# Kernel tuning notes

Measured on AMD Instinct MI355X. Metric: run time of the kernel, lower is better.

## Reference

```python
import jax, jax.numpy as jnp
import numpy as np
from jax import lax

BETA = 1.0
EPS_BIS = 0.1   # eps_threshold of FIND_MIN
N_ITER = 24     # enough bisection steps for any interval width seen here
N_BOX = 2097152
TINY = 1e-12


def _slog(x):
    return jnp.log(jnp.maximum(x, TINY))


def _sl1(x):  # smooth_l1_loss
    d = jnp.abs(x)
    return jnp.where(d < BETA, 0.5 * d * d / BETA, d - 0.5 * BETA)


def _sl1p(x):  # smooth_l1_loss_prime
    return jnp.clip(x / BETA, -1.0, 1.0)


def _xi_prime(w, wp, wh):
    return 0.5 * _sl1p(0.5 * (w - wh)) + _sl1p(_slog(w) - _slog(wp)) / jnp.maximum(w, TINY)


def _sigma(w, wp, wh):
    return w * _xi_prime(w, wp, wh)


def _xi(w, wp, wh):  # bbox_loss at x=(w-wh)/2
    return _sl1(0.5 * (w - wh)) + _sl1(_slog(wp) - _slog(w))


def _bisect(u, v, f):
    # vectorized FIND_MIN: early-exit endpoints + bisection to width < EPS_BIS
    fu, fv = f(u), f(v)

    def body(i, c):
        lo, hi = c
        act = (hi - lo) >= EPS_BIS
        m = 0.5 * (lo + hi)
        pos = f(m) >= 0
        lo = jnp.where(act & ~pos, m, lo)
        hi = jnp.where(act & pos, m, hi)
        return lo, hi

    lo, hi = lax.fori_loop(0, N_ITER, body, (u, v))
    m = 0.5 * (lo + hi)
    return jnp.where(fu >= 0, u, jnp.where(fv <= 0, v, m))


def _solve_o1(wp, wh, a1, b1):
    w0 = b1 - a1
    fxp = lambda w: _xi_prime(w, wp, wh)
    fsg = lambda w: _sigma(w, wp, wh)
    # branch A: max(w0, wh) < wp
    rA = _bisect(jnp.maximum(w0, wh), wp, fxp)
    eb = np.float32(np.exp(BETA))
    emin = np.float32(np.exp(min(BETA, 1.0)))
    e1 = np.float32(np.e)
    base = jnp.maximum(w0, jnp.maximum(wh - 2.0 * BETA, e1 * wp))
    disc = jnp.sqrt(jnp.maximum(1.0 - 32.0 / jnp.maximum(wh * wh, TINY), 0.0))
    r1 = _bisect(jnp.maximum(w0, wp), jnp.minimum(emin * wp, wh), fxp)                 # J1
    r2 = _bisect(jnp.maximum(jnp.maximum(w0, 2.0 * np.sqrt(BETA)),
                             jnp.maximum(wh - 2.0 * BETA, eb * wp)), wh, fxp)          # J2
    r3 = _bisect(base, jnp.minimum(eb, wh), fsg)                                        # J3
    r4 = _bisect(base, jnp.minimum(jnp.minimum(eb * wp, wh), 0.25 * wh * (1 + disc)), fsg)  # J4
    r5 = _bisect(jnp.maximum(base, 0.25 * wh * (1 - disc)), jnp.minimum(eb * wp, wh), fsg)  # J5
    cands = jnp.stack([w0, wh, r1, r2, r3, r4, r5])  # [7, N]
    xis = _xi(cands, wp, wh)
    small = wh <= 4.0 * np.sqrt(2.0)
    inf = jnp.float32(np.inf)
    xis = xis.at[4].set(jnp.where(small, xis[4], inf))  # J3 only when wh <= 4*sqrt(2)
    xis = xis.at[5].set(jnp.where(small, inf, xis[5]))  # J4/J5 otherwise
    xis = xis.at[6].set(jnp.where(small, inf, xis[6]))
    rB = jnp.take_along_axis(cands, jnp.argmin(xis, axis=0)[None], axis=0)[0]
    bA = jnp.maximum(w0, wh) < wp
    bB = jnp.maximum(w0, wp) < wh
    return jnp.where(bA, rA, jnp.where(bB, rB, w0))


def _solve_o2(dp, wp, a2, b2):
    wh1 = 2.0 * (dp - a2)
    wh2 = 2.0 * (b2 - dp)
    w1 = _solve_o1(wp, wh1, a2, b2)
    w2 = _solve_o1(wp, wh2, a2, b2)
    p1 = _xi(w1, wp, wh1) <= _xi(w2, wp, wh2)
    d = jnp.where(p1, a2 + 0.5 * w1, b2 - 0.5 * w2)
    w = jnp.where(p1, w1, w2)
    triv = wp >= jnp.maximum(wh1, wh2)
    return jnp.where(triv, dp, d), jnp.where(triv, wp, w)


def _case_axis(pred, prop, cases, target, crop, axis):
    lt, rb, d, o = (0, 1, 0, 2) if axis == 0 else (2, 3, 1, 3)
    ca = 0.5 * (prop[:, d] + prop[:, o]) + 0.5
    da = prop[:, o] - prop[:, d] + 1.0
    crop_a = crop[:, axis]
    # right/bottom cropped only
    a1r = target[:, d] - 0.5 * target[:, o]
    b1r = (crop_a - ca) / da
    wr = _solve_o1(pred[:, o], 2.0 * (pred[:, d] - a1r), a1r, b1r)
    dr = a1r + 0.5 * wr
    # left/top cropped only
    a1l = -ca / da
    b1l = target[:, d] + 0.5 * target[:, o]
    wl = _solve_o1(pred[:, o], 2.0 * (b1l - pred[:, d]), a1l, b1l)
    dl = b1l - 0.5 * wl
    # both sides cropped
    db, wb = _solve_o2(pred[:, d], pred[:, o], a1l, b1r)
    cl, cr = cases[:, lt], cases[:, rb]
    delta = jnp.where(~cl & ~cr, target[:, d],
            jnp.where(cr & ~cl, dr,
            jnp.where(cl & ~cr, dl, db)))
    omega = jnp.where(~cl & ~cr, target[:, o],
            jnp.where(cr & ~cl, wr,
            jnp.where(cl & ~cr, wl, wb)))
    return delta, omega


def _forward(pred, target, proposal_list, cases, crop_shapes):
    dx, wx = _case_axis(pred, proposal_list, cases, target, crop_shapes, 0)
    dy, wy = _case_axis(pred, proposal_list, cases, target, crop_shapes, 1)
    # torch.tensor(label) detaches -> stop_gradient
    label = lax.stop_gradient(jnp.stack([dx, dy, wx, wy], axis=1))
    return _sl1(pred - label)


def setup_inputs() -> dict:
    key = jax.random.key(0)
    ks = jax.random.split(key, 8)
    N = N_BOX
    deltas = 0.3 * jax.random.normal(ks[0], (N, 2), jnp.float32)
    omegas = jax.random.uniform(ks[1], (N, 2), jnp.float32, 0.5, 3.0)  # omega must be > 0 (log)
    pred = jnp.concatenate([deltas, omegas], axis=1)
    tdel = 0.3 * jax.random.normal(ks[2], (N, 2), jnp.float32)
    tom = jax.random.uniform(ks[3], (N, 2), jnp.float32, 0.5, 2.5)
    target = jnp.concatenate([tdel, tom], axis=1)
    xy1 = jax.random.uniform(ks[4], (N, 2), jnp.float32, 0.0, 800.0)
    wh = jax.random.uniform(ks[5], (N, 2), jnp.float32, 10.0, 110.0)
    proposal_list = jnp.stack([xy1[:, 0], xy1[:, 1], xy1[:, 0] + wh[:, 0], xy1[:, 1] + wh[:, 1]], axis=1)
    cases = jax.random.bernoulli(ks[6], 0.5, (N, 4))
    crop_shapes = jax.random.uniform(ks[7], (N, 2), jnp.float32, 500.0, 1024.0)
    return {"pred": pred, "target": target, "proposal_list": proposal_list,
            "cases": cases, "crop_shapes": crop_shapes}


def reference(pred, target, proposal_list, cases, crop_shapes):
    return _forward(pred, target, proposal_list, cases, crop_shapes)
```

## Files before the change

kernel.cpp:

```cpp
#include <hip/hip_runtime.h>

#define TINYF   1e-12f
#define EPSB    0.1f
#define EULERF  2.7182817f
#define SMALLWH 5.656854249f

__device__ __forceinline__ float clip1(float x) { return fminf(fmaxf(x, -1.0f), 1.0f); }
__device__ __forceinline__ float slogx(float x) { return __logf(fmaxf(x, TINYF)); }
__device__ __forceinline__ float sl1(float x) {
    float d = fabsf(x);
    return d < 1.0f ? 0.5f * d * d : d - 0.5f;
}

__device__ __forceinline__ float heval(float w, float wh, float lwp) {
    float t  = clip1(slogx(w) - lwp);
    float c2 = clip1(0.5f * (w - wh));
    return fmaf(0.5f * c2, fmaxf(w, TINYF), t);
}

__device__ __forceinline__ float xieval(float w, float wh, float lwp) {
    return sl1(0.5f * (w - wh)) + sl1(lwp - slogx(w));
}

__device__ __forceinline__ float bisect(float u, float v, float wh, float lwp) {
    float fu = heval(u, wh, lwp);
    float fv = heval(v, wh, lwp);
    float lo = u, hi = v;
#pragma unroll 1
    for (int it = 0; it < 24; ++it) {
        bool act = (hi - lo) >= EPSB;
        if (!__any(act)) break;
        float m = 0.5f * (lo + hi);
        if (act) {
            if (heval(m, wh, lwp) >= 0.0f) hi = m; else lo = m;
        }
    }
    float m = 0.5f * (lo + hi);
    return (fu >= 0.0f) ? u : ((fv <= 0.0f) ? v : m);
}

__device__ __forceinline__ int classify(float wp, float wh, float w0) {
    bool bA = fmaxf(w0, wh) < wp;
    bool bB = fmaxf(w0, wp) < wh;
    if (bA) return 0;
    if (bB) return (wh <= SMALLWH) ? 1 : 2;
    return 3;
}

__device__ __forceinline__ float solveA(float wp, float wh, float w0, float lwp) {
    return bisect(fmaxf(w0, wh), wp, wh, lwp);
}

__device__ __forceinline__ float solveB(float wp, float wh, float w0, float lwp, bool small) {
    float ewp  = EULERF * wp;
    float base = fmaxf(w0, fmaxf(wh - 2.0f, ewp));
    float r1 = bisect(fmaxf(w0, wp), fminf(ewp, wh), wh, lwp);
    float r2 = bisect(fmaxf(fmaxf(w0, 2.0f), fmaxf(wh - 2.0f, ewp)), wh, wh, lwp);
    float rB = w0, best = xieval(w0, wh, lwp), x;
    x = xieval(wh, wh, lwp); if (x < best) { best = x; rB = wh; }
    x = xieval(r1, wh, lwp); if (x < best) { best = x; rB = r1; }
    x = xieval(r2, wh, lwp); if (x < best) { best = x; rB = r2; }
    if (small) {
        float r3 = bisect(base, fminf(EULERF, wh), wh, lwp);
        x = xieval(r3, wh, lwp); if (x < best) { best = x; rB = r3; }
    } else {
        float disc = sqrtf(fmaxf(1.0f - __fdividef(32.0f, fmaxf(wh * wh, TINYF)), 0.0f));
        float r4 = bisect(base, fminf(fminf(ewp, wh), 0.25f * wh * (1.0f + disc)), wh, lwp);
        float r5 = bisect(fmaxf(base, 0.25f * wh * (1.0f - disc)), fminf(ewp, wh), wh, lwp);
        x = xieval(r4, wh, lwp); if (x < best) { best = x; rB = r4; }
        x = xieval(r5, wh, lwp); if (x < best) { best = x; rB = r5; }
    }
    return rB;
}

__device__ __forceinline__ void load_cases(const void* cases, int flag, int i,
                                           bool& c0, bool& c1, bool& c2, bool& c3) {
    if (flag == 1) {
        int4 ci = ((const int4*)cases)[i];
        c0 = ci.x != 0; c1 = ci.y != 0; c2 = ci.z != 0; c3 = ci.w != 0;
    } else if (flag == 2) {
        float4 cf = ((const float4*)cases)[i];
        c0 = cf.x != 0.0f; c1 = cf.y != 0.0f; c2 = cf.z != 0.0f; c3 = cf.w != 0.0f;
    } else {
        uchar4 cb = ((const uchar4*)cases)[i];
        c0 = cb.x != 0; c1 = cb.y != 0; c2 = cb.z != 0; c3 = cb.w != 0;
    }
}

__global__ void detect_cases_kernel(const unsigned char* __restrict__ cases, int* __restrict__ flag) {
    if (threadIdx.x == 0 && blockIdx.x == 0) {
        bool i32ok = true, f32ok = true;
        for (int g = 0; g < 64; ++g) {
            unsigned char b0 = cases[g * 4 + 0];
            unsigned char b1 = cases[g * 4 + 1];
            unsigned char b2 = cases[g * 4 + 2];
            unsigned char b3 = cases[g * 4 + 3];
            i32ok = i32ok && (b0 <= 1) && (b1 == 0) && (b2 == 0) && (b3 == 0);
            bool zf = (b2 == 0 && b3 == 0);
            bool of = (b2 == 0x80 && b3 == 0x3f);
            f32ok = f32ok && (b0 == 0) && (b1 == 0) && (zf || of);
        }
        *flag = i32ok ? 1 : (f32ok ? 2 : 0);
    }
}

__global__ __launch_bounds__(256) void cabb_fused(
        const float4* __restrict__ pred4, const float4* __restrict__ targ4,
        const float4* __restrict__ prop4, const void* __restrict__ cases,
        const float2* __restrict__ crop2, const int* __restrict__ flagp,
        float4* __restrict__ out4, int n) {
    __shared__ float tWp[1024], tWh[1024], tW0[1024];
    __shared__ unsigned short tDst[1024];
    __shared__ float resW[1024];
    __shared__ int cnt[3];
    __shared__ int base[3];

    int tid = threadIdx.x;
    int i = blockIdx.x * 256 + tid;
    if (tid < 3) cnt[tid] = 0;
    __syncthreads();

    bool valid = i < n;
    float4 pr = {0,0,0,0}, tg = {0,0,0,0};
    float caA[2] = {0,0}, daA[2] = {1,1}, cropA[2] = {0,0};
    bool clA[2] = {false,false}, crA[2] = {false,false};

    float sWp[4], sWh[4], sW0[4];
    int sCls[4], sPos[4];
#pragma unroll
    for (int k = 0; k < 4; ++k) { sCls[k] = -1; sPos[k] = 0; sWp[k] = 0; sWh[k] = 0; sW0[k] = 0; }

    if (valid) {
        pr = pred4[i]; tg = targ4[i];
        float4 pp = prop4[i];
        float2 cs = crop2[i];
        bool c0, c1, c2, c3;
        load_cases(cases, *flagp, i, c0, c1, c2, c3);
        clA[0] = c0; crA[0] = c1; clA[1] = c2; crA[1] = c3;
        caA[0] = 0.5f * (pp.x + pp.z) + 0.5f;  daA[0] = pp.z - pp.x + 1.0f;  cropA[0] = cs.x;
        caA[1] = 0.5f * (pp.y + pp.w) + 0.5f;  daA[1] = pp.w - pp.y + 1.0f;  cropA[1] = cs.y;
    }

#pragma unroll
    for (int axis = 0; axis < 2; ++axis) {
        if (!valid) continue;
        bool L = clA[axis], R = crA[axis];
        if (!(L || R)) continue;
        float pd = axis ? pr.y : pr.x, po = axis ? pr.w : pr.z;
        float td = axis ? tg.y : tg.x, to = axis ? tg.w : tg.z;
        int k0 = axis * 2, k1 = axis * 2 + 1;
        if (R && !L) {
            float a1 = td - 0.5f * to;
            float b1 = __fdividef(cropA[axis] - caA[axis], daA[axis]);
            float wh = 2.0f * (pd - a1), w0 = b1 - a1;
            int c = classify(po, wh, w0);
            if (c == 3) resW[(tid << 2) | (axis << 1)] = w0;
            else { sCls[k0] = c; sWp[k0] = po; sWh[k0] = wh; sW0[k0] = w0; }
        } else if (L && !R) {
            float a1 = __fdividef(-caA[axis], daA[axis]);
            float b1 = td + 0.5f * to;
            float wh = 2.0f * (b1 - pd), w0 = b1 - a1;
            int c = classify(po, wh, w0);
            if (c == 3) resW[(tid << 2) | (axis << 1)] = w0;
            else { sCls[k0] = c; sWp[k0] = po; sWh[k0] = wh; sW0[k0] = w0; }
        } else {
            float a1l = __fdividef(-caA[axis], daA[axis]);
            float b1r = __fdividef(cropA[axis] - caA[axis], daA[axis]);
            float wh1 = 2.0f * (pd - a1l), wh2 = 2.0f * (b1r - pd);
            if (po < fmaxf(wh1, wh2)) {
                float w0 = b1r - a1l;
                int ck0 = classify(po, wh1, w0);
                if (ck0 == 3) resW[(tid << 2) | (axis << 1)] = w0;
                else { sCls[k0] = ck0; sWp[k0] = po; sWh[k0] = wh1; sW0[k0] = w0; }
                int ck1 = classify(po, wh2, w0);
                if (ck1 == 3) resW[(tid << 2) | (axis << 1) | 1] = w0;
                else { sCls[k1] = ck1; sWp[k1] = po; sWh[k1] = wh2; sW0[k1] = w0; }
            }
        }
    }

#pragma unroll
    for (int k = 0; k < 4; ++k) {
#pragma unroll
        for (int c = 0; c < 3; ++c) {
            bool mine = (sCls[k] == c);
            unsigned long long mask = __ballot(mine);
            if (mine) {
                int lane = tid & 63;
                int off = (int)__popcll(mask & ((1ull << lane) - 1ull));
                int leader = (int)__ffsll((unsigned long long)mask) - 1;
                int wb = 0;
                if (lane == leader) wb = atomicAdd(&cnt[c], (int)__popcll(mask));
                wb = __shfl(wb, leader);
                sPos[k] = wb + off;
            }
        }
    }
    __syncthreads();
    if (tid == 0) { base[0] = 0; base[1] = cnt[0]; base[2] = cnt[0] + cnt[1]; }
    __syncthreads();
#pragma unroll
    for (int k = 0; k < 4; ++k) {
        if (sCls[k] >= 0) {
            int p = base[sCls[k]] + sPos[k];
            tWp[p] = sWp[k]; tWh[p] = sWh[k]; tW0[p] = sW0[k];
            tDst[p] = (unsigned short)((tid << 2) | k);
        }
    }
    __syncthreads();

    int nA = base[1], nAB1 = base[2], total = base[2] + cnt[2];
    for (int t0 = 0; t0 < total; t0 += 256) {
        int t = t0 + tid;
        if (t < total) {
            float wp = tWp[t], wh = tWh[t], w0 = tW0[t];
            float lwp = __logf(fmaxf(wp, TINYF));
            float w;
            if (t < nA) w = solveA(wp, wh, w0, lwp);
            else        w = solveB(wp, wh, w0, lwp, t < nAB1);
            resW[tDst[t]] = w;
        }
    }
    __syncthreads();

    if (valid) {
        float labd[2], labw[2];
#pragma unroll
        for (int axis = 0; axis < 2; ++axis) {
            bool L = clA[axis], R = crA[axis];
            float pd = axis ? pr.y : pr.x, po = axis ? pr.w : pr.z;
            float td = axis ? tg.y : tg.x, to = axis ? tg.w : tg.z;
            float delta, omega;
            if (!L && !R) { delta = td; omega = to; }
            else if (R && !L) {
                float w = resW[(tid << 2) | (axis << 1)];
                float a1 = td - 0.5f * to;
                delta = a1 + 0.5f * w; omega = w;
            } else if (L && !R) {
                float w = resW[(tid << 2) | (axis << 1)];
                float b1 = td + 0.5f * to;
                delta = b1 - 0.5f * w; omega = w;
            } else {
                float a1l = __fdividef(-caA[axis], daA[axis]);
                float b1r = __fdividef(cropA[axis] - caA[axis], daA[axis]);
                float wh1 = 2.0f * (pd - a1l), wh2 = 2.0f * (b1r - pd);
                if (po >= fmaxf(wh1, wh2)) { delta = pd; omega = po; }
                else {
                    float w1 = resW[(tid << 2) | (axis << 1)];
                    float w2 = resW[(tid << 2) | (axis << 1) | 1];
                    float lwp = __logf(fmaxf(po, TINYF));
                    bool p1 = xieval(w1, wh1, lwp) <= xieval(w2, wh2, lwp);
                    delta = p1 ? (a1l + 0.5f * w1) : (b1r - 0.5f * w2);
                    omega = p1 ? w1 : w2;
                }
            }
            labd[axis] = delta; labw[axis] = omega;
        }
        float4 o;
        o.x = sl1(pr.x - labd[0]);
        o.y = sl1(pr.y - labd[1]);
        o.z = sl1(pr.z - labw[0]);
        o.w = sl1(pr.w - labw[1]);
        out4[i] = o;
    }
}

extern "C" void kernel_launch(void* const* d_in, const int* in_sizes, int n_in,
                              void* d_out, int out_size, void* d_ws, size_t ws_size,
                              hipStream_t stream) {
    const float4* pred = (const float4*)d_in[0];
    const float4* targ = (const float4*)d_in[1];
    const float4* prop = (const float4*)d_in[2];
    const void*   cases = d_in[3];
    const float2* crop = (const float2*)d_in[4];
    float4* out = (float4*)d_out;
    int n = in_sizes[0] / 4;
    int* flag = (int*)d_ws;

    detect_cases_kernel<<<1, 64, 0, stream>>>((const unsigned char*)cases, flag);
    int nb = (n + 255) / 256;
    cabb_fused<<<nb, 256, 0, stream>>>(pred, targ, prop, cases, crop, flag, out, n);
}
```

Before: 196.6 us.

## Fold case-dtype detection into main kernel and simplify shared-memory compaction

Removes the separate single-thread detection launch and instead has the first wave of every block detect the cases dtype with ballots. This drops one kernel launch and the serialized dependency on it. It also switches the resW/tDst slot layout from interleaved per-thread to slot-major, which avoids shared-memory bank conflicts. Per-wave ballot compaction is replaced with plain per-thread LDS atomics. Each block now redundantly reads 256 bytes, and LDS atomic contention may increase.

Measured after the change: 188.7 us. -4.0%, faster.

```diff
diff --git a/kernel.cpp b/kernel.cpp
--- a/kernel.cpp
+++ b/kernel.cpp
@@ -87,38 +87,33 @@
     }
 }
 
-__global__ void detect_cases_kernel(const unsigned char* __restrict__ cases, int* __restrict__ flag) {
-    if (threadIdx.x == 0 && blockIdx.x == 0) {
-        bool i32ok = true, f32ok = true;
-        for (int g = 0; g < 64; ++g) {
-            unsigned char b0 = cases[g * 4 + 0];
-            unsigned char b1 = cases[g * 4 + 1];
-            unsigned char b2 = cases[g * 4 + 2];
-            unsigned char b3 = cases[g * 4 + 3];
-            i32ok = i32ok && (b0 <= 1) && (b1 == 0) && (b2 == 0) && (b3 == 0);
-            bool zf = (b2 == 0 && b3 == 0);
-            bool of = (b2 == 0x80 && b3 == 0x3f);
-            f32ok = f32ok && (b0 == 0) && (b1 == 0) && (zf || of);
-        }
-        *flag = i32ok ? 1 : (f32ok ? 2 : 0);
-    }
-}
-
 __global__ __launch_bounds__(256) void cabb_fused(
         const float4* __restrict__ pred4, const float4* __restrict__ targ4,
         const float4* __restrict__ prop4, const void* __restrict__ cases,
-        const float2* __restrict__ crop2, const int* __restrict__ flagp,
+        const float2* __restrict__ crop2,
         float4* __restrict__ out4, int n) {
     __shared__ float tWp[1024], tWh[1024], tW0[1024];
     __shared__ unsigned short tDst[1024];
     __shared__ float resW[1024];
     __shared__ int cnt[3];
     __shared__ int base[3];
+    __shared__ int sFlag;
 
     int tid = threadIdx.x;
     int i = blockIdx.x * 256 + tid;
     if (tid < 3) cnt[tid] = 0;
-    __syncthreads();
+
+    if (tid < 64) {
+        uchar4 cb = ((const uchar4*)cases)[tid];
+        bool i32ok = (cb.x <= 1) && (cb.y == 0) && (cb.z == 0) && (cb.w == 0);
+        bool f32ok = (cb.x == 0) && (cb.y == 0) &&
+                     ((cb.z == 0 && cb.w == 0) || (cb.z == 0x80 && cb.w == 0x3f));
+        unsigned long long m32 = __ballot(i32ok);
+        unsigned long long mf  = __ballot(f32ok);
+        if (tid == 0) sFlag = (m32 == ~0ull) ? 1 : ((mf == ~0ull) ? 2 : 0);
+    }
+    __syncthreads();
+    int flag = sFlag;
 
     bool valid = i < n;
     float4 pr = {0,0,0,0}, tg = {0,0,0,0};
@@ -135,7 +130,7 @@
         float4 pp = prop4[i];
         float2 cs = crop2[i];
         bool c0, c1, c2, c3;
-        load_cases(cases, *flagp, i, c0, c1, c2, c3);
+        load_cases(cases, flag, i, c0, c1, c2, c3);
         clA[0] = c0; crA[0] = c1; clA[1] = c2; crA[1] = c3;
         caA[0] = 0.5f * (pp.x + pp.z) + 0.5f;  daA[0] = pp.z - pp.x + 1.0f;  cropA[0] = cs.x;
         caA[1] = 0.5f * (pp.y + pp.w) + 0.5f;  daA[1] = pp.w - pp.y + 1.0f;  cropA[1] = cs.y;
@@ -154,14 +149,14 @@
             float b1 = __fdividef(cropA[axis] - caA[axis], daA[axis]);
             float wh = 2.0f * (pd - a1), w0 = b1 - a1;
             int c = classify(po, wh, w0);
-            if (c == 3) resW[(tid << 2) | (axis << 1)] = w0;
+            if (c == 3) resW[k0 * 256 + tid] = w0;
             else { sCls[k0] = c; sWp[k0] = po; sWh[k0] = wh; sW0[k0] = w0; }
         } else if (L && !R) {
             float a1 = __fdividef(-caA[axis], daA[axis]);
             float b1 = td + 0.5f * to;
             float wh = 2.0f * (b1 - pd), w0 = b1 - a1;
             int c = classify(po, wh, w0);
-            if (c == 3) resW[(tid << 2) | (axis << 1)] = w0;
+            if (c == 3) resW[k0 * 256 + tid] = w0;
             else { sCls[k0] = c; sWp[k0] = po; sWh[k0] = wh; sW0[k0] = w0; }
         } else {
             float a1l = __fdividef(-caA[axis], daA[axis]);
@@ -170,10 +165,10 @@
             if (po < fmaxf(wh1, wh2)) {
                 float w0 = b1r - a1l;
                 int ck0 = classify(po, wh1, w0);
-                if (ck0 == 3) resW[(tid << 2) | (axis << 1)] = w0;
+                if (ck0 == 3) resW[k0 * 256 + tid] = w0;
                 else { sCls[k0] = ck0; sWp[k0] = po; sWh[k0] = wh1; sW0[k0] = w0; }
                 int ck1 = classify(po, wh2, w0);
-                if (ck1 == 3) resW[(tid << 2) | (axis << 1) | 1] = w0;
+                if (ck1 == 3) resW[k1 * 256 + tid] = w0;
                 else { sCls[k1] = ck1; sWp[k1] = po; sWh[k1] = wh2; sW0[k1] = w0; }
             }
         }
@@ -181,20 +176,7 @@
 
 #pragma unroll
     for (int k = 0; k < 4; ++k) {
-#pragma unroll
-        for (int c = 0; c < 3; ++c) {
-            bool mine = (sCls[k] == c);
-            unsigned long long mask = __ballot(mine);
-            if (mine) {
-                int lane = tid & 63;
-                int off = (int)__popcll(mask & ((1ull << lane) - 1ull));
-                int leader = (int)__ffsll((unsigned long long)mask) - 1;
-                int wb = 0;
-                if (lane == leader) wb = atomicAdd(&cnt[c], (int)__popcll(mask));
-                wb = __shfl(wb, leader);
-                sPos[k] = wb + off;
-            }
-        }
+        if (sCls[k] >= 0) sPos[k] = atomicAdd(&cnt[sCls[k]], 1);
     }
     __syncthreads();
     if (tid == 0) { base[0] = 0; base[1] = cnt[0]; base[2] = cnt[0] + cnt[1]; }
@@ -204,7 +186,7 @@
         if (sCls[k] >= 0) {
             int p = base[sCls[k]] + sPos[k];
             tWp[p] = sWp[k]; tWh[p] = sWh[k]; tW0[p] = sW0[k];
-            tDst[p] = (unsigned short)((tid << 2) | k);
+            tDst[p] = (unsigned short)(k * 256 + tid);
         }
     }
     __syncthreads();
@@ -233,11 +215,11 @@
             float delta, omega;
             if (!L && !R) { delta = td; omega = to; }
             else if (R && !L) {
-                float w = resW[(tid << 2) | (axis << 1)];
+                float w = resW[(axis * 2) * 256 + tid];
                 float a1 = td - 0.5f * to;
                 delta = a1 + 0.5f * w; omega = w;
             } else if (L && !R) {
-                float w = resW[(tid << 2) | (axis << 1)];
+                float w = resW[(axis * 2) * 256 + tid];
                 float b1 = td + 0.5f * to;
                 delta = b1 - 0.5f * w; omega = w;
             } else {
@@ -246,8 +228,8 @@
                 float wh1 = 2.0f * (pd - a1l), wh2 = 2.0f * (b1r - pd);
                 if (po >= fmaxf(wh1, wh2)) { delta = pd; omega = po; }
                 else {
-                    float w1 = resW[(tid << 2) | (axis << 1)];
-                    float w2 = resW[(tid << 2) | (axis << 1) | 1];
+                    float w1 = resW[(axis * 2) * 256 + tid];
+                    float w2 = resW[(axis * 2 + 1) * 256 + tid];
                     float lwp = __logf(fmaxf(po, TINYF));
                     bool p1 = xieval(w1, wh1, lwp) <= xieval(w2, wh2, lwp);
                     delta = p1 ? (a1l + 0.5f * w1) : (b1r - 0.5f * w2);
@@ -275,9 +257,7 @@
     const float2* crop = (const float2*)d_in[4];
     float4* out = (float4*)d_out;
     int n = in_sizes[0] / 4;
-    int* flag = (int*)d_ws;
-
-    detect_cases_kernel<<<1, 64, 0, stream>>>((const unsigned char*)cases, flag);
+
     int nb = (n + 255) / 256;
-    cabb_fused<<<nb, 256, 0, stream>>>(pred, targ, prop, cases, crop, flag, out, n);
-}
+    cabb_fused<<<nb, 256, 0, stream>>>(pred, targ, prop, cases, crop, out, n);
+}
```
